# Optimization experiments

Measured on AMD Instinct MI355X. Metric: run time of the kernel, lower is better.

## Reference

```python
import jax, jax.numpy as jnp
import numpy as np

N = 16384
E = 524288
D_IN = 256
D_OUT = 256


def setup_inputs() -> dict:
    key = jax.random.key(0)
    k1, k2, k3, k4, k5, k6 = jax.random.split(key, 6)
    x = jax.random.normal(k1, (N, D_IN), dtype=jnp.float32)
    edge_index = jax.random.randint(k2, (2, E), 0, N, dtype=jnp.int64)
    W_update = jax.random.normal(k3, (D_OUT, D_IN), dtype=jnp.float32) / np.sqrt(D_IN)
    b_update = jax.random.normal(k4, (D_OUT,), dtype=jnp.float32) * 0.01
    W_aggregate = jax.random.normal(k5, (D_OUT, D_IN), dtype=jnp.float32) / np.sqrt(D_IN)
    b_aggregate = jax.random.normal(k6, (D_OUT,), dtype=jnp.float32) * 0.01
    return {
        "x": x,
        "edge_index": edge_index,
        "W_update": W_update,
        "b_update": b_update,
        "W_aggregate": W_aggregate,
        "b_aggregate": b_aggregate,
    }


def reference(x, edge_index, W_update, b_update, W_aggregate, b_aggregate):
    n = x.shape[0]
    src, dst = edge_index[0], edge_index[1]
    # Dense symmetric 0/1 adjacency built with SET semantics (duplicate edges
    # contribute 1, not their count) -- faithful to the torch indexing assign.
    adj = jnp.zeros((n, n), dtype=x.dtype)
    adj = adj.at[src, dst].set(1.0)
    adj = adj.at[dst, src].set(1.0)
    messages = adj @ x                                   # [N, D_in]
    aggregated = messages @ W_aggregate.T + b_aggregate  # [N, D_out]
    updated = x @ W_update.T + b_update + aggregated     # [N, D_out]
    return updated
```

## Files before the change

### kernel.cpp

```cpp
#include <hip/hip_runtime.h>
#include <hip/hip_fp16.h>

#define NN 16384
#define DD 256
#define CAP 160
#define NB 128
#define BK 64
#define LDAP 72
#define PLP 2099200
#define XUP 2097152

typedef __attribute__((ext_vector_type(8))) __bf16 bf16x8;
typedef __attribute__((ext_vector_type(8))) unsigned short u16x8;
typedef __attribute__((ext_vector_type(4))) float f32x4;

__device__ __forceinline__ unsigned short f2bn(float f) {
    __bf16 h = (__bf16)f;
    return __builtin_bit_cast(unsigned short, h);
}

__global__ __launch_bounds__(512) void k_prep(const int* __restrict__ ei,
                                              unsigned int* __restrict__ Hc,
                                              const float* __restrict__ x,
                                              const float* __restrict__ Wu,
                                              const float* __restrict__ Wa,
                                              unsigned short* __restrict__ xb,
                                              unsigned short* __restrict__ wb,
                                              __half* __restrict__ xab,
                                              int E, int epb) {
    const int b = blockIdx.x;
    const int t = threadIdx.x;

    if (b >= 128) {
        if (b < 192) {
            const int w = b - 128;
#pragma unroll
            for (int i = 0; i < 32; ++i) {
                const int f4 = w * 16384 + i * 512 + t;
                float4 v = *(const float4*)(x + (size_t)f4 * 4);
                ushort4 o;
                o.x = f2bn(v.x); o.y = f2bn(v.y); o.z = f2bn(v.z); o.w = f2bn(v.w);
                *(ushort4*)(xb + (size_t)f4 * 4) = o;
            }
        } else if (b < 200) {
            const int w = b - 192;
            const float* src = (w < 4) ? Wu : Wa;
            unsigned short* dst = wb + ((w < 4) ? 0 : 65536);
            const int c0 = (w & 3) * 4096;
#pragma unroll
            for (int i = 0; i < 8; ++i) {
                const int f4 = c0 + i * 512 + t;
                float4 v = *(const float4*)(src + (size_t)f4 * 4);
                ushort4 o;
                o.x = f2bn(v.x); o.y = f2bn(v.y); o.z = f2bn(v.z); o.w = f2bn(v.w);
                *(ushort4*)(dst + (size_t)f4 * 4) = o;
            }
        } else {
            uint4 z; z.x = 0u; z.y = 0u; z.z = 0u; z.w = 0u;
            ((uint4*)xab)[(size_t)(t >> 8) * (PLP / 8) + (NN * 128 / 8) + (t & 255)] = z;
        }
        return;
    }

    __shared__ unsigned int hc[128];
    if (t < 128) hc[t] = 0u;
    __syncthreads();

    const int e0 = b * epb;
    const int e1 = min(e0 + epb, E);
    for (int e = e0 + t; e < e1; e += 512) {
        const int s = ei[e];
        const int d = ei[E + e];
        atomicAdd(&hc[s >> 7], 1u);
        atomicAdd(&hc[d >> 7], 1u);
    }
    __syncthreads();
    if (t < 128) Hc[b * 128 + t] = hc[t];
}

__global__ __launch_bounds__(512) void k_scan1(const unsigned int* __restrict__ Hc,
                                               unsigned int* __restrict__ runOfs,
                                               unsigned int* __restrict__ bstart) {
    __shared__ unsigned short h16[128 * 128];
    __shared__ unsigned int tot[128];
    __shared__ unsigned int bs[129];
    const int t = threadIdx.x;

    for (int i = t; i < 128 * 128; i += 512) h16[i] = (unsigned short)Hc[i];
    __syncthreads();

    if (t < 128) {
        unsigned int s = 0;
#pragma unroll 8
        for (int b = 0; b < 128; ++b) {
            const unsigned int v = h16[b * 128 + t];
            h16[b * 128 + t] = (unsigned short)s;
            s += v;
        }
        tot[t] = s;
    }
    __syncthreads();
    if (t == 0) {
        unsigned int s = 0;
        for (int k = 0; k < 128; ++k) { bs[k] = s; s += tot[k]; }
        bs[128] = s;
    }
    __syncthreads();

    for (int i = t; i < 128 * 128; i += 512)
        runOfs[i] = bs[i & 127] + (unsigned int)h16[i];
    if (t < 129) bstart[t] = bs[t];
}

__global__ __launch_bounds__(512) void k_gemm_fill1(const unsigned short* __restrict__ xb,
                                                    const unsigned short* __restrict__ wb,
                                                    const float* __restrict__ bu,
                                                    const float* __restrict__ ba,
                                                    const int* __restrict__ ei,
                                                    const unsigned int* __restrict__ runOfs,
                                                    unsigned int* __restrict__ edgebuf,
                                                    __half* __restrict__ xu,
                                                    __half* __restrict__ xab,
                                                    int E, int epb) {
    __shared__ __align__(16) unsigned short smem[2 * 128 * LDAP];
    const int t = threadIdx.x;

    if (blockIdx.x >= 512) {
        unsigned int* cur = (unsigned int*)smem;
        const int b = blockIdx.x - 512;
        if (t < 128) cur[t] = runOfs[b * 128 + t];
        __syncthreads();
        const int e0 = b * epb;
        const int e1 = min(e0 + epb, E);
        for (int e = e0 + t; e < e1; e += 512) {
            const unsigned int s = (unsigned int)ei[e];
            const unsigned int d = (unsigned int)ei[E + e];
            const unsigned int p1 = atomicAdd(&cur[s >> 7], 1u);
            edgebuf[p1] = (s << 14) | d;
            const unsigned int p2 = atomicAdd(&cur[d >> 7], 1u);
            edgebuf[p2] = (d << 14) | s;
        }
        return;
    }

    unsigned short* As = smem;
    unsigned short* Bs = smem + 128 * LDAP;

    const int lane = t & 63;
    const int wid = t >> 6;
    const int wr = wid >> 2;
    const int wc = wid & 3;
    const int rowp = blockIdx.x & 127;
    const int colq = blockIdx.x >> 7;
    const int row0 = rowp << 7;
    const unsigned short* Wsrc = wb + ((size_t)colq << 15);

    f32x4 acc[4][2] = {};

    for (int k0 = 0; k0 < DD; k0 += BK) {
        uint4 ra_[2], rb_[2];
#pragma unroll
        for (int i = 0; i < 2; ++i) {
            const int f = i * 512 + t;
            const int r = f >> 3, s = f & 7;
            ra_[i] = *(const uint4*)(xb + (size_t)(row0 + r) * DD + k0 + s * 8);
            rb_[i] = *(const uint4*)(Wsrc + (size_t)r * DD + k0 + s * 8);
        }
        __syncthreads();
#pragma unroll
        for (int i = 0; i < 2; ++i) {
            const int f = i * 512 + t;
            const int r = f >> 3, s = f & 7;
            *(uint4*)(&As[r * LDAP + s * 8]) = ra_[i];
            *(uint4*)(&Bs[r * LDAP + s * 8]) = rb_[i];
        }
        __syncthreads();
#pragma unroll
        for (int kk = 0; kk < 2; ++kk) {
            bf16x8 av[4], bv[2];
#pragma unroll
            for (int f = 0; f < 4; ++f) {
                uint4 ra = *(const uint4*)(&As[(wr * 64 + f * 16 + (lane & 15)) * LDAP + kk * 32 + (lane >> 4) * 8]);
                av[f] = __builtin_bit_cast(bf16x8, ra);
            }
#pragma unroll
            for (int f = 0; f < 2; ++f) {
                uint4 rv = *(const uint4*)(&Bs[(wc * 32 + f * 16 + (lane & 15)) * LDAP + kk * 32 + (lane >> 4) * 8]);
                bv[f] = __builtin_bit_cast(bf16x8, rv);
            }
#pragma unroll
            for (int fm = 0; fm < 4; ++fm)
#pragma unroll
                for (int fn = 0; fn < 2; ++fn)
                    acc[fm][fn] = __builtin_amdgcn_mfma_f32_16x16x32_bf16(
                        av[fm], bv[fn], acc[fm][fn], 0, 0, 0);
        }
    }

    const int gr0 = row0 + wr * 64 + ((lane >> 4) << 2);
    const int lc0 = wc * 32 + (lane & 15);
    if (colq < 2) {
        __half* up = xu + (size_t)colq * XUP;
#pragma unroll
        for (int fn = 0; fn < 2; ++fn) {
            const int c = lc0 + fn * 16;
            const float bias = bu[(colq << 7) + c] + ba[(colq << 7) + c];
#pragma unroll
            for (int fm = 0; fm < 4; ++fm) {
                const int r = gr0 + fm * 16;
#pragma unroll
                for (int i = 0; i < 4; ++i)
                    up[(size_t)(r + i) * 128 + c] = __float2half(acc[fm][fn][i] + bias);
            }
        }
    } else {
        __half* xp = xab + (size_t)(colq - 2) * PLP;
#pragma unroll
        for (int fn = 0; fn < 2; ++fn) {
            const int c = lc0 + fn * 16;
#pragma unroll
            for (int fm = 0; fm < 4; ++fm) {
                const int r = gr0 + fm * 16;
#pragma unroll
                for (int i = 0; i < 4; ++i)
                    xp[(size_t)(r + i) * 128 + c] = __float2half(acc[fm][fn][i]);
            }
        }
    }
}

__global__ __launch_bounds__(512) void k_fill2(const unsigned int* __restrict__ edgebuf,
                                               const unsigned int* __restrict__ bstart,
                                               unsigned short* __restrict__ list,
                                               unsigned int* __restrict__ cnt) {
    __shared__ unsigned short ll[128 * CAP];
    __shared__ unsigned int cur[128];
    const int k = blockIdx.x;
    const int t = threadIdx.x;

    if (t < 128) cur[t] = 0u;
    {
        u16x8 s8;
#pragma unroll
        for (int j = 0; j < 8; ++j) s8[j] = (unsigned short)NN;
        for (int i = t; i < 128 * CAP / 8; i += 512) *(u16x8*)(ll + i * 8) = s8;
    }
    __syncthreads();

    const unsigned int s0 = bstart[k], s1 = bstart[k + 1];
    for (unsigned int j = s0 + t; j < s1; j += 512) {
        const unsigned int e = edgebuf[j];
        const int lr = (int)((e >> 14) & 127u);
        const unsigned short nbr = (unsigned short)(e & 16383u);
        const unsigned int p = atomicAdd(&cur[lr], 1u);
        if (p < CAP) ll[lr * CAP + p] = nbr;
    }
    __syncthreads();

    const int lr = t >> 2;
    const int sub = t & 3;
    const unsigned int padded = min((cur[lr] + 31u) & ~31u, (unsigned int)CAP);
    if (sub == 0) cnt[(k << 7) + lr] = padded;
    unsigned short* lrow = list + (size_t)((k << 7) + lr) * CAP;
    for (unsigned int q = sub; q * 8 < padded; q += 4)
        *(u16x8*)(lrow + q * 8) = *(const u16x8*)(ll + lr * CAP + q * 8);
}

#define ACC4(S, V) { \
    acc[S][0] = __hadd2(acc[S][0], __builtin_bit_cast(__half2, (V).x)); \
    acc[S][1] = __hadd2(acc[S][1], __builtin_bit_cast(__half2, (V).y)); \
    acc[S][2] = __hadd2(acc[S][2], __builtin_bit_cast(__half2, (V).z)); \
    acc[S][3] = __hadd2(acc[S][3], __builtin_bit_cast(__half2, (V).w)); }

__global__ __launch_bounds__(256) void k_gather(const unsigned int* __restrict__ cnt,
                                                const unsigned short* __restrict__ list,
                                                const __half* __restrict__ plane,
                                                const __half* __restrict__ uplane,
                                                float* __restrict__ out,
                                                int outoff) {
    __shared__ unsigned int bmw[4][512];
    __shared__ unsigned short lst[4][CAP];

    const int t = threadIdx.x;
    const int wid = t >> 6;
    const int lane = t & 63;
    const int row = (blockIdx.x << 2) + wid;

    uint4 z4; z4.x = 0u; z4.y = 0u; z4.z = 0u; z4.w = 0u;
    ((uint4*)&bmw[wid][0])[lane] = z4;
    ((uint4*)&bmw[wid][0])[64 + lane] = z4;

    const int m = min((int)cnt[row], CAP);
    const unsigned short* gl = list + (size_t)row * CAP;
    for (int i = lane; i < m; i += 64) {
        int idx = gl[i];
        if (idx < NN) {
            const unsigned int bit = 1u << (idx & 31);
            const unsigned int old = atomicOr(&bmw[wid][idx >> 5], bit);
            if (old & bit) idx = NN;
        }
        lst[wid][i] = (unsigned short)idx;
    }

    const int lg = lane >> 4;
    const int li = lane & 15;
    __half2 acc[4][4];
    const __half2 z2 = __float2half2_rn(0.0f);
#pragma unroll
    for (int s = 0; s < 4; ++s) { acc[s][0] = z2; acc[s][1] = z2; acc[s][2] = z2; acc[s][3] = z2; }

    int i = 0;
    for (; i + 32 <= m; i += 32) {
        const u16x8 e = *(const u16x8*)(&lst[wid][i + lg * 8]);
        uint4 v[8];
#pragma unroll
        for (int j = 0; j < 8; ++j)
            v[j] = *(const uint4*)(plane + ((size_t)e[j] << 7) + li * 8);
#pragma unroll
        for (int j = 0; j < 8; ++j) ACC4(j & 3, v[j]);
    }

#pragma unroll
    for (int k = 0; k < 4; ++k) {
        acc[0][k] = __hadd2(acc[0][k], __hadd2(acc[1][k], __hadd2(acc[2][k], acc[3][k])));
        int v = __builtin_bit_cast(int, acc[0][k]);
        v = __shfl_xor(v, 16, 64);
        acc[0][k] = __hadd2(acc[0][k], __builtin_bit_cast(__half2, v));
        v = __builtin_bit_cast(int, acc[0][k]);
        v = __shfl_xor(v, 32, 64);
        acc[0][k] = __hadd2(acc[0][k], __builtin_bit_cast(__half2, v));
    }

    if (lg == 0) {
        const uint4 u = *(const uint4*)(uplane + (size_t)row * 128 + li * 8);
        float4 o0, o1;
        float2 f, g;
        f = __half22float2(acc[0][0]); g = __half22float2(__builtin_bit_cast(__half2, u.x));
        o0.x = f.x + g.x; o0.y = f.y + g.y;
        f = __half22float2(acc[0][1]); g = __half22float2(__builtin_bit_cast(__half2, u.y));
        o0.z = f.x + g.x; o0.w = f.y + g.y;
        f = __half22float2(acc[0][2]); g = __half22float2(__builtin_bit_cast(__half2, u.z));
        o1.x = f.x + g.x; o1.y = f.y + g.y;
        f = __half22float2(acc[0][3]); g = __half22float2(__builtin_bit_cast(__half2, u.w));
        o1.z = f.x + g.x; o1.w = f.y + g.y;
        float4* po = (float4*)(out + (size_t)row * DD + outoff + li * 8);
        po[0] = o0; po[1] = o1;
    }
}

extern "C" void kernel_launch(void* const* d_in, const int* in_sizes, int n_in,
                              void* d_out, int out_size, void* d_ws, size_t ws_size,
                              hipStream_t stream) {
    const float* x  = (const float*)d_in[0];
    const int*   ei = (const int*)d_in[1];
    const float* Wu = (const float*)d_in[2];
    const float* bu = (const float*)d_in[3];
    const float* Wa = (const float*)d_in[4];
    const float* ba = (const float*)d_in[5];
    float* out = (float*)d_out;

    const int E = in_sizes[1] / 2;
    const int epb = (E + NB - 1) / NB;

    char* ws = (char*)d_ws;
    __half* xab = (__half*)ws;
    __half* xu = (__half*)(ws + 8396800);
    unsigned short* wb = (unsigned short*)(ws + 16785408);
    unsigned short* xb = (unsigned short*)(ws + 17047552);
    unsigned int* Hc = (unsigned int*)(ws + 25436160);
    unsigned int* runOfs = (unsigned int*)(ws + 25501696);
    unsigned int* bstart = (unsigned int*)(ws + 25567232);
    unsigned int* edgebuf = (unsigned int*)(ws + 25568256);
    unsigned int* cnt = (unsigned int*)(ws + 29762560);
    unsigned short* list = (unsigned short*)(ws + 29828096);

    k_prep<<<201, 512, 0, stream>>>(ei, Hc, x, Wu, Wa, xb, wb, xab, E, epb);
    k_scan1<<<1, 512, 0, stream>>>(Hc, runOfs, bstart);
    k_gemm_fill1<<<640, 512, 0, stream>>>(xb, wb, bu, ba, ei, runOfs, edgebuf, xu, xab, E, epb);
    k_fill2<<<NB, 512, 0, stream>>>(edgebuf, bstart, list, cnt);
    k_gather<<<NN / 4, 256, 0, stream>>>(cnt, list, xab, xu, out, 0);
    k_gather<<<NN / 4, 256, 0, stream>>>(cnt, list, xab + PLP, xu + XUP, out, 128);
}
```

Measured before the change: 92.43 us.

## Move neighbor dedup into fill kernel and merge two gather launches

Duplicate-neighbor removal moves out of the gather kernel and into k_fill2. It runs once per row with a shared-memory bitmap and marks duplicates with the sentinel index. Before, this work ran twice, once per column-half gather. The two gather launches become one launch of twice the grid, with the half selected by block index. The gather now reads the neighbor list straight from global memory without staging it in LDS. In exchange, k_fill2 gains a serial per-warp dedup loop and 16KB more shared memory, which may lower its occupancy.

```diff
diff --git a/kernel.cpp b/kernel.cpp
--- a/kernel.cpp
+++ b/kernel.cpp
@@ -234,9 +234,12 @@
                                                unsigned short* __restrict__ list,
                                                unsigned int* __restrict__ cnt) {
     __shared__ unsigned short ll[128 * CAP];
+    __shared__ unsigned int dbm[8][512];
     __shared__ unsigned int cur[128];
     const int k = blockIdx.x;
     const int t = threadIdx.x;
+    const int w = t >> 6;
+    const int lane = t & 63;
 
     if (t < 128) cur[t] = 0u;
     {
@@ -257,6 +260,21 @@
     }
     __syncthreads();
 
+    uint4 z4; z4.x = 0u; z4.y = 0u; z4.z = 0u; z4.w = 0u;
+    for (int rr = 0; rr < 16; ++rr) {
+        const int lr = (w << 4) + rr;
+        ((uint4*)&dbm[w][0])[lane] = z4;
+        ((uint4*)&dbm[w][0])[64 + lane] = z4;
+        const int m = min((int)cur[lr], CAP);
+        for (int i = lane; i < m; i += 64) {
+            const int idx = ll[lr * CAP + i];
+            const unsigned int bit = 1u << (idx & 31);
+            const unsigned int old = atomicOr(&dbm[w][idx >> 5], bit);
+            if (old & bit) ll[lr * CAP + i] = (unsigned short)NN;
+        }
+    }
+    __syncthreads();
+
     const int lr = t >> 2;
     const int sub = t & 3;
     const unsigned int padded = min((cur[lr] + 31u) & ~31u, (unsigned int)CAP);
@@ -274,33 +292,19 @@
 
 __global__ __launch_bounds__(256) void k_gather(const unsigned int* __restrict__ cnt,
                                                 const unsigned short* __restrict__ list,
-                                                const __half* __restrict__ plane,
-                                                const __half* __restrict__ uplane,
-                                                float* __restrict__ out,
-                                                int outoff) {
-    __shared__ unsigned int bmw[4][512];
-    __shared__ unsigned short lst[4][CAP];
-
+                                                const __half* __restrict__ xab,
+                                                const __half* __restrict__ xu,
+                                                float* __restrict__ out) {
     const int t = threadIdx.x;
     const int wid = t >> 6;
     const int lane = t & 63;
-    const int row = (blockIdx.x << 2) + wid;
-
-    uint4 z4; z4.x = 0u; z4.y = 0u; z4.z = 0u; z4.w = 0u;
-    ((uint4*)&bmw[wid][0])[lane] = z4;
-    ((uint4*)&bmw[wid][0])[64 + lane] = z4;
-
-    const int m = min((int)cnt[row], CAP);
+    const int pb = blockIdx.x >> 12;
+    const int row = ((blockIdx.x & 4095) << 2) + wid;
+    const __half* plane = xab + (size_t)pb * PLP;
+    const __half* uplane = xu + (size_t)pb * XUP;
+
+    const int m = (int)cnt[row];
     const unsigned short* gl = list + (size_t)row * CAP;
-    for (int i = lane; i < m; i += 64) {
-        int idx = gl[i];
-        if (idx < NN) {
-            const unsigned int bit = 1u << (idx & 31);
-            const unsigned int old = atomicOr(&bmw[wid][idx >> 5], bit);
-            if (old & bit) idx = NN;
-        }
-        lst[wid][i] = (unsigned short)idx;
-    }
 
     const int lg = lane >> 4;
     const int li = lane & 15;
@@ -309,9 +313,8 @@
 #pragma unroll
     for (int s = 0; s < 4; ++s) { acc[s][0] = z2; acc[s][1] = z2; acc[s][2] = z2; acc[s][3] = z2; }
 
-    int i = 0;
-    for (; i + 32 <= m; i += 32) {
-        const u16x8 e = *(const u16x8*)(&lst[wid][i + lg * 8]);
+    for (int i = 0; i < m; i += 32) {
+        const u16x8 e = *(const u16x8*)(gl + i + lg * 8);
         uint4 v[8];
 #pragma unroll
         for (int j = 0; j < 8; ++j)
@@ -343,7 +346,7 @@
         o1.x = f.x + g.x; o1.y = f.y + g.y;
         f = __half22float2(acc[0][3]); g = __half22float2(__builtin_bit_cast(__half2, u.w));
         o1.z = f.x + g.x; o1.w = f.y + g.y;
-        float4* po = (float4*)(out + (size_t)row * DD + outoff + li * 8);
+        float4* po = (float4*)(out + (size_t)row * DD + (pb << 7) + li * 8);
         po[0] = o0; po[1] = o1;
     }
 }
@@ -378,6 +381,5 @@
     k_scan1<<<1, 512, 0, stream>>>(Hc, runOfs, bstart);
     k_gemm_fill1<<<640, 512, 0, stream>>>(xb, wb, bu, ba, ei, runOfs, edgebuf, xu, xab, E, epb);
     k_fill2<<<NB, 512, 0, stream>>>(edgebuf, bstart, list, cnt);
-    k_gather<<<NN / 4, 256, 0, stream>>>(cnt, list, xab, xu, out, 0);
-    k_gather<<<NN / 4, 256, 0, stream>>>(cnt, list, xab + PLP, xu + XUP, out, 128);
-}
+    k_gather<<<2 * (NN / 4), 256, 0, stream>>>(cnt, list, xab, xu, out);
+}
```

After: 93.97 us. Within noise of the previous version (+1.7%).
